# Optimization experiments

Hardware: AMD Instinct MI355X
Metric: run time of the kernel (lower is better)

The kernel has to match this reference:

```python
import jax, jax.numpy as jnp
import numpy as np

B, T, V, S, I, G = 2, 4096, 1024, 256, 2048, 128


def setup_inputs() -> dict:
    key = jax.random.key(0)
    ks = jax.random.split(key, 10)
    n = lambda k, shape, std: jax.random.normal(k, shape, dtype=jnp.float32) * std
    return {
        "x": jax.random.normal(ks[0], (B, T, V), dtype=jnp.float32),
        # shared CausalMemory projections (torch Linear weight layout [out,in])
        "Wq": n(ks[1], (S, V), 0.02),
        "Wk": n(ks[2], (S, V), 0.02),
        "Wv": n(ks[3], (S, V), 0.02),
        "Wo": n(ks[4], (V, S), 0.02),
        # Delta
        "delta_logits": jnp.full((V,), 4.0, dtype=jnp.float32),
        "delta_scale": jnp.float32(0.1),
        # Theta / Gamma decay params
        "theta_decay": jnp.float32(4.0),
        "theta_scale": jnp.float32(0.1),
        "gamma_decay": jnp.float32(1.0),
        "gamma_scale": jnp.float32(0.1),
        # Alpha gate
        "alpha_down": n(ks[5], (G, V), 0.02),
        "alpha_up": n(ks[6], (V, G), 0.01),
        "alpha_up_b": jnp.full((V,), 2.0, dtype=jnp.float32),
        # Beta MLP
        "beta_down": n(ks[7], (I, V), 0.02),
        "beta_up": n(ks[8], (V, I), 0.02),
        "beta_bias": jnp.zeros((I,), dtype=jnp.float32),
        "beta_scale": jnp.float32(0.1),
    }


def _rmsnorm(x):
    eps = jnp.finfo(x.dtype).eps
    return x * jax.lax.rsqrt(jnp.mean(x * x, axis=-1, keepdims=True) + eps)


def _delta(x, decay_logits, scale):
    # causal EMA via weighted cumsum, matching torch reference exactly
    t = x.shape[1]
    decay = jax.nn.sigmoid(decay_logits)
    log_decay = jnp.log(jnp.clip(decay, 1e-06))
    steps = jnp.arange(t, dtype=x.dtype)[::-1]            # [T]
    w = jnp.exp(steps[:, None] * log_decay[None, :])      # [T,V]
    cum = jnp.cumsum(x * w[None], axis=1)
    cum = jnp.concatenate([jnp.zeros_like(cum[:, :1]), cum[:, :-1]], axis=1)
    return cum / jnp.clip(w[None], 1e-08) * scale


def _memory(x, Wq, Wk, Wv, Wo, decay_logit, scale):
    t = x.shape[1]
    q = x @ Wq.T
    k = x @ Wk.T
    v = x @ Wv.T
    scores = jnp.einsum("btd,bsd->bts", q, k)             # [B,T,T]
    decay = jax.nn.sigmoid(decay_logit)
    pos = jnp.arange(t)
    diff = pos[None, :] - pos[:, None]                    # j - i
    w = decay ** jnp.clip(diff.astype(x.dtype) - 1.0, 0.0, None) * (diff > 0)
    retrieved = jnp.einsum("bts,bsd->btd", scores * w[None], v)
    return (retrieved @ Wo.T) * scale


def _alpha(x, down, up, up_b):
    gate = jax.nn.sigmoid((x @ down.T) @ up.T + up_b)
    return x * gate


def _beta(x, down, up, bias, scale):
    h = jax.nn.gelu(x @ down.T + bias, approximate=False)
    return (h @ up.T) * scale


def reference(x, Wq, Wk, Wv, Wo, delta_logits, delta_scale, theta_decay,
              theta_scale, gamma_decay, gamma_scale, alpha_down, alpha_up,
              alpha_up_b, beta_down, beta_up, beta_bias, beta_scale):
    x = x + _delta(_rmsnorm(x), delta_logits, delta_scale)
    x = x + _memory(_rmsnorm(x), Wq, Wk, Wv, Wo, theta_decay, theta_scale)
    x = _alpha(x, alpha_down, alpha_up, alpha_up_b)
    x = x + _beta(_rmsnorm(x), beta_down, beta_up, beta_bias, beta_scale)
    x = x + _memory(_rmsnorm(x), Wq, Wk, Wv, Wo, gamma_decay, gamma_scale)
    return x
```

## Files before the change

kernel.cpp:

```cpp
#include <hip/hip_runtime.h>

typedef __attribute__((ext_vector_type(8))) short s16x8;
typedef __attribute__((ext_vector_type(4))) float f32x4;
typedef unsigned short u16;

#define DEV __device__ __forceinline__

DEV u16 f2b(float f) {
  unsigned u = __builtin_bit_cast(unsigned, f);
  unsigned r = (u + 0x7FFFu + ((u >> 16) & 1u)) >> 16;
  return (u16)r;
}
DEV float b2f(u16 h) { return __builtin_bit_cast(float, (unsigned)h << 16); }
DEV f32x4 mfma16(s16x8 a, s16x8 b, f32x4 c) {
  return __builtin_amdgcn_mfma_f32_16x16x32_bf16(a, b, c, 0, 0, 0);
}
DEV float sigmoidf_(float x) { return 1.0f / (1.0f + expf(-x)); }

DEV void g2l16(const u16* g, u16* l) {
  __builtin_amdgcn_global_load_lds((const __attribute__((address_space(1))) void*)g,
                                   (__attribute__((address_space(3))) void*)l, 16, 0, 0);
}

#define BAR() __builtin_amdgcn_s_barrier()
#define WAITV8() asm volatile("s_waitcnt vmcnt(8)" ::: "memory")
#define WAITV4() asm volatile("s_waitcnt vmcnt(4)" ::: "memory")
#define WAITV0() asm volatile("s_waitcnt vmcnt(0)" ::: "memory")
#define WAITL0()                                         \
  do {                                                   \
    asm volatile("s_waitcnt lgkmcnt(0)" ::: "memory");   \
    __builtin_amdgcn_sched_barrier(0);                   \
  } while (0)

__global__ __launch_bounds__(256) void cast_all(
    const float* __restrict__ Wq, const float* __restrict__ Wk, const float* __restrict__ Wv,
    const float* __restrict__ Wo, const float* __restrict__ adw, const float* __restrict__ auw,
    const float* __restrict__ bdw, const float* __restrict__ buw,
    u16* __restrict__ Wqkvb, u16* __restrict__ Wob, u16* __restrict__ adb,
    u16* __restrict__ aub, u16* __restrict__ bdb, u16* __restrict__ bub) {
  const int b = blockIdx.x;
  const float* s;
  u16* d;
  int rb;
  if (b < 768) {
    s = (b < 256) ? Wq : (b < 512) ? Wk : Wv;
    rb = (b < 256) ? b : (b < 512) ? (b - 256) : (b - 512);
    d = Wqkvb + ((b < 256) ? 0 : (b < 512) ? 262144 : 524288);
  } else if (b < 1024) { s = Wo;  d = Wob; rb = b - 768; }
  else if (b < 1152)   { s = adw; d = adb; rb = b - 1024; }
  else if (b < 1280)   { s = auw; d = aub; rb = b - 1152; }
  else if (b < 3328)   { s = bdw; d = bdb; rb = b - 1280; }
  else                 { s = buw; d = bub; rb = b - 3328; }
  size_t i = ((size_t)rb * 256 + threadIdx.x) * 4;
  float4 v = *(const float4*)(s + i);
  ushort4 p; p.x = f2b(v.x); p.y = f2b(v.y); p.z = f2b(v.z); p.w = f2b(v.w);
  *(ushort4*)(d + i) = p;
}

__global__ __launch_bounds__(256) void rmsnorm_k(const float* __restrict__ x, u16* __restrict__ y) {
  const size_t row = blockIdx.x;
  const int tid = threadIdx.x;
  float4 v = ((const float4*)(x + row * 1024))[tid];
  float ss = v.x * v.x + v.y * v.y + v.z * v.z + v.w * v.w;
#pragma unroll
  for (int o = 32; o >= 1; o >>= 1) ss += __shfl_xor(ss, o);
  __shared__ float red[4];
  if ((tid & 63) == 0) red[tid >> 6] = ss;
  __syncthreads();
  float tot = red[0] + red[1] + red[2] + red[3];
  float rn = rsqrtf(tot * (1.0f / 1024.0f) + 1.1920929e-7f);
  ushort4 p;
  p.x = f2b(v.x * rn); p.y = f2b(v.y * rn); p.z = f2b(v.z * rn); p.w = f2b(v.w * rn);
  *(ushort4*)(y + row * 1024 + tid * 4) = p;
}

__global__ __launch_bounds__(256)
void delta_partial(const u16* __restrict__ y, const float* __restrict__ logits, float* __restrict__ Pp) {
  const int v = blockIdx.x * 256 + threadIdx.x;
  const int c = blockIdx.y, b = blockIdx.z;
  const float dec = sigmoidf_(logits[v]);
  const float ldc = logf(fmaxf(dec, 1e-6f));
  const u16* yp = y + ((size_t)b * 4096 + c * 128) * 1024 + v;
  float acc = 0.0f;
  for (int t = 0; t < 128; ++t) {
    float wgt = expf((float)(4095 - (c * 128 + t)) * ldc);
    acc += b2f(yp[(size_t)t * 1024]) * wgt;
  }
  Pp[((size_t)b * 32 + c) * 1024 + v] = acc;
}

__global__ __launch_bounds__(256) void delta_scan(float* __restrict__ Pp) {
  const int v = blockIdx.x * 256 + threadIdx.x;
  const int b = blockIdx.y;
  float run = 0.0f;
  for (int c = 0; c < 32; ++c) {
    size_t i = ((size_t)b * 32 + c) * 1024 + v;
    float t = Pp[i];
    Pp[i] = run;
    run += t;
  }
}

__global__ __launch_bounds__(256)
void delta_apply(const float* __restrict__ x0, const u16* __restrict__ y,
                 const float* __restrict__ logits, const float* __restrict__ scale_p,
                 const float* __restrict__ Pp, float* __restrict__ x1) {
  const int v = blockIdx.x * 256 + threadIdx.x;
  const int c = blockIdx.y, b = blockIdx.z;
  const float dec = sigmoidf_(logits[v]);
  const float ldc = logf(fmaxf(dec, 1e-6f));
  const float sc = scale_p[0];
  float carry = Pp[((size_t)b * 32 + c) * 1024 + v];
  size_t base = ((size_t)b * 4096 + c * 128) * 1024 + v;
  for (int t = 0; t < 128; ++t) {
    float wgt = expf((float)(4095 - (c * 128 + t)) * ldc);
    size_t idx = base + (size_t)t * 1024;
    x1[idx] = x0[idx] + carry / fmaxf(wgt, 1e-8f) * sc;
    carry += b2f(y[idx]) * wgt;
  }
}

template <int EPI>
__global__ __launch_bounds__(256, 2)
void pgemm(const u16* __restrict__ A, const u16* __restrict__ Bw,
           int M, int N, int K,
           u16* __restrict__ Cb,
           const float* __restrict__ Xin, float* __restrict__ Xout,
           u16* __restrict__ Xb16,
           const float* __restrict__ bias, const float* __restrict__ scale_p,
           u16* __restrict__ P1, u16* __restrict__ P2, u16* __restrict__ P3) {
  __shared__ u16 sm[32768];
  const int tid = threadIdx.x;
  const int wid = tid >> 6, lane = tid & 63;
  const int gx = gridDim.x;
  const int id = blockIdx.y * gx + blockIdx.x;
  const int q8 = (gx * gridDim.y) >> 3;
  const int nid = (id & 7) * q8 + (id >> 3);
  const int bx = nid % gx, by = nid / gx;
  const int n0 = bx * 128, m0 = by * 128;
  const int wm = (wid >> 1) * 64, wn = (wid & 1) * 64;
  const int lr = lane & 15, lkc = lane >> 4;
  const int sw = lr & 7;
  const int c0 = (lkc ^ sw) * 8, c1 = ((lkc + 4) ^ sw) * 8;
  const int NT = K >> 6;
  const int srow = lane >> 3;
  const int scol = ((lane & 7) ^ srow) * 8;
  const u16* Ag = A + (size_t)(m0 + wid * 8 + srow) * K + scol;
  const u16* Bg = Bw + (size_t)(n0 + wid * 8 + srow) * K + scol;
  u16* const AL0 = sm;          u16* const BL0 = sm + 8192;
  u16* const AL1 = sm + 16384;  u16* const BL1 = sm + 24576;

  f32x4 acc[4][4] = {};

  auto STA = [&](int tau) {
    const u16* g = Ag + (size_t)tau * 64;
    u16* l = ((tau & 1) ? AL1 : AL0) + wid * 512;
#pragma unroll
    for (int c = 0; c < 4; ++c) g2l16(g + (size_t)c * 32 * K, l + c * 2048);
  };
  auto STB = [&](int tau) {
    const u16* g = Bg + (size_t)tau * 64;
    u16* l = ((tau & 1) ? BL1 : BL0) + wid * 512;
#pragma unroll
    for (int c = 0; c < 4; ++c) g2l16(g + (size_t)c * 32 * K, l + c * 2048);
  };
  auto RDA = [&](int tau, s16x8 (&d)[4][2]) {
    const u16* Ab = (tau & 1) ? AL1 : AL0;
#pragma unroll
    for (int i = 0; i < 4; ++i) {
      int base = (wm + i * 16 + lr) * 64;
      d[i][0] = *(const s16x8*)&Ab[base + c0];
      d[i][1] = *(const s16x8*)&Ab[base + c1];
    }
  };
  auto RDB = [&](int tau, int h, s16x8 (&d)[2][2]) {
    const u16* Bb = (tau & 1) ? BL1 : BL0;
#pragma unroll
    for (int j = 0; j < 2; ++j) {
      int base = (wn + h * 32 + j * 16 + lr) * 64;
      d[j][0] = *(const s16x8*)&Bb[base + c0];
      d[j][1] = *(const s16x8*)&Bb[base + c1];
    }
  };
  auto MM = [&](s16x8 (&Ar)[4][2], s16x8 (&Br)[2][2], int jo) {
    __builtin_amdgcn_s_setprio(1);
#pragma unroll
    for (int i = 0; i < 4; ++i)
#pragma unroll
      for (int j = 0; j < 2; ++j) {
        acc[i][jo + j] = mfma16(Ar[i][0], Br[j][0], acc[i][jo + j]);
        acc[i][jo + j] = mfma16(Ar[i][1], Br[j][1], acc[i][jo + j]);
      }
    __builtin_amdgcn_s_setprio(0);
  };

  s16x8 Ae[4][2], Ao[4][2], B0r[2][2], B1r[2][2];
  STA(0); STB(0);
  if (NT > 1) { STA(1); STB(1); }
  WAITV8(); BAR();
  RDA(0, Ae); RDB(0, 0, B0r);

  for (int t = 0; t < NT; t += 2) {
    RDB(t, 1, B1r);
    if (t + 2 < NT) STA(t + 2);
    BAR(); WAITL0();
    MM(Ae, B0r, 0);
    BAR();
    if (t + 2 < NT) { STB(t + 2); WAITV8(); } else { WAITV0(); }
    BAR();
    if (t + 1 < NT) { RDA(t + 1, Ao); RDB(t + 1, 0, B0r); }
    WAITL0();
    MM(Ae, B1r, 2);
    BAR();
    if (t + 1 >= NT) break;
    RDB(t + 1, 1, B1r);
    if (t + 3 < NT) STA(t + 3);
    BAR(); WAITL0();
    MM(Ao, B0r, 0);
    BAR();
    if (t + 3 < NT) { STB(t + 3); WAITV8(); } else { WAITV0(); }
    BAR();
    if (t + 2 < NT) { RDA(t + 2, Ae); RDB(t + 2, 0, B0r); }
    WAITL0();
    MM(Ao, B1r, 2);
    BAR();
  }

  float* tl = (float*)(void*)sm + wid * 1088;

  if constexpr (EPI == 5) {
    if (bx < 4) {
      u16* dst = (bx < 2) ? Cb : P1;
      const int nb = (bx & 1) * 128;
#pragma unroll
      for (int i = 0; i < 4; ++i) {
#pragma unroll
        for (int j = 0; j < 4; ++j)
#pragma unroll
          for (int r = 0; r < 4; ++r)
            tl[(lkc * 4 + r) * 68 + j * 16 + lr] = acc[i][j][r];
#pragma unroll
        for (int p = 0; p < 4; ++p) {
          const int row = p * 4 + lkc, nl = lr * 4;
          f32x4 v = *(const f32x4*)&tl[row * 68 + nl];
          const int m = m0 + wm + i * 16 + row;
          ushort4 o = {f2b(v[0]), f2b(v[1]), f2b(v[2]), f2b(v[3])};
          *(ushort4*)&dst[(size_t)m * 256 + nb + wn + nl] = o;
        }
      }
      if (bx >= 2) {
        const float ld5 = logf(sigmoidf_(scale_p[0]));
        u16* CT = sm;
        __syncthreads();
#pragma unroll
        for (int i = 0; i < 4; ++i)
#pragma unroll
          for (int j = 0; j < 4; ++j)
#pragma unroll
            for (int r = 0; r < 4; ++r) {
              int ml = wm + i * 16 + lkc * 4 + r;
              int nl = wn + j * 16 + lr;
              float g = expf(ld5 * (float)(ml & 63));
              CT[nl * 136 + ml] = f2b(acc[i][j][r] * g);
            }
        __syncthreads();
        int d = tid >> 1, off = (tid & 1) * 64;
        size_t base = ((size_t)(m0 >> 12) * 256 + (bx - 2) * 128 + d) * 4096 + (m0 & 4095) + off;
#pragma unroll
        for (int p = 0; p < 8; ++p)
          *(uint4*)&P3[base + p * 8] = *(const uint4*)&CT[d * 136 + off + p * 8];
      }
    } else {
      u16* CT = sm;
      __syncthreads();
#pragma unroll
      for (int i = 0; i < 4; ++i)
#pragma unroll
        for (int j = 0; j < 4; ++j)
#pragma unroll
          for (int r = 0; r < 4; ++r) {
            int ml = wm + i * 16 + lkc * 4 + r;
            int nl = wn + j * 16 + lr;
            CT[nl * 136 + ml] = f2b(acc[i][j][r]);
          }
      __syncthreads();
      int d = tid >> 1, off = (tid & 1) * 64;
      size_t base = ((size_t)(m0 >> 12) * 256 + (bx - 4) * 128 + d) * 4096 + (m0 & 4095) + off;
#pragma unroll
      for (int p = 0; p < 8; ++p)
        *(uint4*)&P2[base + p * 8] = *(const uint4*)&CT[d * 136 + off + p * 8];
    }
  } else {
    const float sc = (EPI == 2) ? scale_p[0] : 0.0f;
#pragma unroll
    for (int i = 0; i < 4; ++i) {
#pragma unroll
      for (int j = 0; j < 4; ++j)
#pragma unroll
        for (int r = 0; r < 4; ++r)
          tl[(lkc * 4 + r) * 68 + j * 16 + lr] = acc[i][j][r];
#pragma unroll
      for (int p = 0; p < 4; ++p) {
        const int row = p * 4 + lkc, nl = lr * 4;
        f32x4 v = *(const f32x4*)&tl[row * 68 + nl];
        const int m = m0 + wm + i * 16 + row;
        const int n = n0 + wn + nl;
        const size_t idx = (size_t)m * N + n;
        if constexpr (EPI == 0) {
          ushort4 o = {f2b(v[0]), f2b(v[1]), f2b(v[2]), f2b(v[3])};
          *(ushort4*)&Cb[idx] = o;
        } else if constexpr (EPI == 2) {
          float4 x = *(const float4*)&Xin[idx];
          float4 o = {x.x + v[0] * sc, x.y + v[1] * sc, x.z + v[2] * sc, x.w + v[3] * sc};
          *(float4*)&Xout[idx] = o;
          if (Xb16) {
            ushort4 ob = {f2b(o.x), f2b(o.y), f2b(o.z), f2b(o.w)};
            *(ushort4*)&Xb16[idx] = ob;
          }
        } else if constexpr (EPI == 3) {
          float4 bb = *(const float4*)&bias[n];
          float g0 = v[0] + bb.x, g1 = v[1] + bb.y, g2 = v[2] + bb.z, g3 = v[3] + bb.w;
          ushort4 o;
          o.x = f2b(g0 * sigmoidf_(1.59576912f * fmaf(0.044715f * g0, g0 * g0, g0)));
          o.y = f2b(g1 * sigmoidf_(1.59576912f * fmaf(0.044715f * g1, g1 * g1, g1)));
          o.z = f2b(g2 * sigmoidf_(1.59576912f * fmaf(0.044715f * g2, g2 * g2, g2)));
          o.w = f2b(g3 * sigmoidf_(1.59576912f * fmaf(0.044715f * g3, g3 * g3, g3)));
          *(ushort4*)&Cb[idx] = o;
        } else {
          float4 bb = *(const float4*)&bias[n];
          float4 x = *(const float4*)&Xin[idx];
          float4 o = {x.x * sigmoidf_(v[0] + bb.x), x.y * sigmoidf_(v[1] + bb.y),
                      x.z * sigmoidf_(v[2] + bb.z), x.w * sigmoidf_(v[3] + bb.w)};
          *(float4*)&Xout[idx] = o;
        }
      }
    }
  }
}

__global__ __launch_bounds__(256, 2)
void chunk_G(const u16* __restrict__ vT, const u16* __restrict__ kTs, float* __restrict__ Gp) {
  __shared__ u16 sm2[16384];
  const int c = blockIdx.x, eh = blockIdx.y >> 1, dh = blockIdx.y & 1, b = blockIdx.z;
  const int tid = threadIdx.x, wid = tid >> 6, lane = tid & 63;
  u16* AL = sm2; u16* BL = sm2 + 8192;
  const u16* As = vT + (size_t)(b * 256 + eh * 128) * 4096 + c * 64;
  const u16* Bs = kTs + (size_t)(b * 256 + dh * 128) * 4096 + c * 64;
  const int r8 = lane >> 3, sc8 = ((lane & 7) ^ (lane >> 3)) * 8;
#pragma unroll
  for (int p = 0; p < 4; ++p) {
    int ch = p * 4 + wid;
    int row = ch * 8 + r8;
    g2l16(As + (size_t)row * 4096 + sc8, AL + ch * 512);
    g2l16(Bs + (size_t)row * 4096 + sc8, BL + ch * 512);
  }
  __syncthreads();
  const int wm = (wid >> 1) * 64, wn = (wid & 1) * 64;
  const int lr = lane & 15, lkc = lane >> 4, sw = lr & 7;
  const int c0 = (lkc ^ sw) * 8, c1 = ((lkc + 4) ^ sw) * 8;
  s16x8 af[4][2], bf[4][2];
#pragma unroll
  for (int i = 0; i < 4; ++i) {
    int ba = (wm + i * 16 + lr) * 64;
    af[i][0] = *(const s16x8*)&AL[ba + c0];
    af[i][1] = *(const s16x8*)&AL[ba + c1];
    int bb = (wn + i * 16 + lr) * 64;
    bf[i][0] = *(const s16x8*)&BL[bb + c0];
    bf[i][1] = *(const s16x8*)&BL[bb + c1];
  }
  f32x4 acc[4][4] = {};
#pragma unroll
  for (int i = 0; i < 4; ++i)
#pragma unroll
    for (int j = 0; j < 4; ++j) {
      acc[i][j] = mfma16(af[i][0], bf[j][0], acc[i][j]);
      acc[i][j] = mfma16(af[i][1], bf[j][1], acc[i][j]);
    }
  float* Gb = Gp + (size_t)(b * 64 + c) * 65536;
#pragma unroll
  for (int i = 0; i < 4; ++i)
#pragma unroll
    for (int j = 0; j < 4; ++j)
#pragma unroll
      for (int r = 0; r < 4; ++r) {
        int e = eh * 128 + wm + i * 16 + lkc * 4 + r;
        int d = dh * 128 + wn + j * 16 + lr;
        Gb[(size_t)e * 256 + d] = acc[i][j][r];
      }
}

__global__ __launch_bounds__(256)
void scan_M(const float* __restrict__ Gp, u16* __restrict__ Mb, const float* __restrict__ dlogit) {
  const int b = blockIdx.y;
  const size_t idx = ((size_t)blockIdx.x * 256 + threadIdx.x) * 4;
  const float ld = logf(sigmoidf_(dlogit[0]));
  const float g64 = expf(64.0f * ld);
  const float* G = Gp + (size_t)b * 64 * 65536 + idx;
  u16* M = Mb + (size_t)b * 64 * 65536 + idx;
  float4 m = {0.0f, 0.0f, 0.0f, 0.0f};
  *(ushort4*)(M + (size_t)63 * 65536) = (ushort4){0, 0, 0, 0};
  float4 g = *(const float4*)(G + (size_t)63 * 65536);
  for (int c = 62; c >= 0; --c) {
    float4 gn = {0.0f, 0.0f, 0.0f, 0.0f};
    if (c > 0) gn = *(const float4*)(G + (size_t)c * 65536);
    m.x = g.x + g64 * m.x; m.y = g.y + g64 * m.y;
    m.z = g.z + g64 * m.z; m.w = g.w + g64 * m.w;
    ushort4 o; o.x = f2b(m.x); o.y = f2b(m.y); o.z = f2b(m.z); o.w = f2b(m.w);
    *(ushort4*)(M + (size_t)c * 65536) = o;
    g = gn;
  }
}

__global__ __launch_bounds__(256, 2)
void chunk_R(const u16* __restrict__ q, const u16* __restrict__ k,
             const u16* __restrict__ vT, const u16* __restrict__ Mb,
             u16* __restrict__ R, const float* __restrict__ dlogit) {
  __shared__ u16 qL[16384];
  __shared__ u16 shA[16384];
  const int c = blockIdx.x, eh = blockIdx.y, b = blockIdx.z;
  const int tid = threadIdx.x, wid = tid >> 6, lane = tid & 63;
  const float ld = logf(sigmoidf_(dlogit[0]));
  const int r8 = lane >> 3, sc8 = ((lane & 7) ^ (lane >> 3)) * 8;
  const int lr = lane & 15, lkc = lane >> 4, g4 = lkc * 4;
  const int sw = lr & 7;
  const int c0 = (lkc ^ sw) * 8, c1 = ((lkc + 4) ^ sw) * 8;

  const u16* qsrc = q + ((size_t)b * 4096 + c * 64) * 256;
  const u16* ksrc = k + ((size_t)b * 4096 + c * 64) * 256;
  const u16* msrc = Mb + ((size_t)(b * 64 + c) * 256 + eh * 128) * 256;
  const u16* vsrc = vT + (size_t)(b * 256 + eh * 128) * 4096 + c * 64;

#pragma unroll
  for (int kt = 0; kt < 4; ++kt)
#pragma unroll
    for (int p = 0; p < 2; ++p) {
      int ch = p * 4 + wid;
      int row = ch * 8 + r8;
      g2l16(qsrc + (size_t)row * 256 + kt * 64 + sc8, qL + kt * 4096 + ch * 512);
    }
#pragma unroll
  for (int p = 0; p < 4; ++p) {
    int ch = p * 4 + wid;
    int row = ch * 8 + r8;
    g2l16(msrc + (size_t)row * 256 + sc8, shA + ch * 512);
  }
  f32x4 accx[4][2] = {};
  for (int dt = 0; dt < 4; ++dt) {
    if (dt < 3) {
      u16* dst = shA + ((dt + 1) & 1) * 8192;
#pragma unroll
      for (int p = 0; p < 4; ++p) {
        int ch = p * 4 + wid;
        int row = ch * 8 + r8;
        g2l16(msrc + (size_t)row * 256 + (dt + 1) * 64 + sc8, dst + ch * 512);
      }
      WAITV4();
    } else {
      WAITV0();
    }
    BAR();
    const u16* mt = shA + (dt & 1) * 8192;
    const u16* qt = qL + dt * 4096;
    s16x8 aq[4][2], bm[2][2];
#pragma unroll
    for (int i = 0; i < 4; ++i) {
      int ba = (i * 16 + lr) * 64;
      aq[i][0] = *(const s16x8*)&qt[ba + c0];
      aq[i][1] = *(const s16x8*)&qt[ba + c1];
    }
#pragma unroll
    for (int j = 0; j < 2; ++j) {
      int ba = (wid * 32 + j * 16 + lr) * 64;
      bm[j][0] = *(const s16x8*)&mt[ba + c0];
      bm[j][1] = *(const s16x8*)&mt[ba + c1];
    }
#pragma unroll
    for (int i = 0; i < 4; ++i)
#pragma unroll
      for (int j = 0; j < 2; ++j) {
        accx[i][j] = mfma16(aq[i][0], bm[j][0], accx[i][j]);
        accx[i][j] = mfma16(aq[i][1], bm[j][1], accx[i][j]);
      }
    BAR();
  }
#pragma unroll
  for (int kt = 0; kt < 4; ++kt)
#pragma unroll
    for (int p = 0; p < 2; ++p) {
      int ch = p * 4 + wid;
      int row = ch * 8 + r8;
      g2l16(ksrc + (size_t)row * 256 + kt * 64 + sc8, shA + kt * 4096 + ch * 512);
    }
  __syncthreads();
  f32x4 accs[4] = {};
#pragma unroll
  for (int kt = 0; kt < 4; ++kt) {
    const u16* qt = qL + kt * 4096;
    const u16* klt = shA + kt * 4096;
    s16x8 aq[4][2], bk[2];
#pragma unroll
    for (int i = 0; i < 4; ++i) {
      int ba = (i * 16 + lr) * 64;
      aq[i][0] = *(const s16x8*)&qt[ba + c0];
      aq[i][1] = *(const s16x8*)&qt[ba + c1];
    }
    {
      int ba = (wid * 16 + lr) * 64;
      bk[0] = *(const s16x8*)&klt[ba + c0];
      bk[1] = *(const s16x8*)&klt[ba + c1];
    }
#pragma unroll
    for (int i = 0; i < 4; ++i) {
      accs[i] = mfma16(aq[i][0], bk[0], accs[i]);
      accs[i] = mfma16(aq[i][1], bk[1], accs[i]);
    }
  }
  __syncthreads();
  u16* PL = shA;
  u16* vTL = shA + 4608;
#pragma unroll
  for (int p = 0; p < 4; ++p) {
    int ch = p * 4 + wid;
    int row = ch * 8 + r8;
    g2l16(vsrc + (size_t)row * 4096 + sc8, vTL + ch * 512);
  }
#pragma unroll
  for (int i = 0; i < 4; ++i)
#pragma unroll
    for (int r = 0; r < 4; ++r) {
      int gi = i * 16 + g4 + r;
      int gj = wid * 16 + lr;
      float pw = (gj > gi) ? expf(ld * (float)(gj - gi - 1)) : 0.0f;
      PL[gi * 72 + gj] = f2b(accs[i][r] * pw);
    }
  __syncthreads();
  f32x4 acci[4][2] = {};
  {
    s16x8 pa[4][2], bv[2][2];
#pragma unroll
    for (int i = 0; i < 4; ++i) {
      pa[i][0] = *(const s16x8*)&PL[(i * 16 + lr) * 72 + lkc * 8];
      pa[i][1] = *(const s16x8*)&PL[(i * 16 + lr) * 72 + 32 + lkc * 8];
    }
#pragma unroll
    for (int j = 0; j < 2; ++j) {
      int ba = (wid * 32 + j * 16 + lr) * 64;
      bv[j][0] = *(const s16x8*)&vTL[ba + c0];
      bv[j][1] = *(const s16x8*)&vTL[ba + c1];
    }
#pragma unroll
    for (int i = 0; i < 4; ++i)
#pragma unroll
      for (int j = 0; j < 2; ++j) {
        acci[i][j] = mfma16(pa[i][0], bv[j][0], acci[i][j]);
        acci[i][j] = mfma16(pa[i][1], bv[j][1], acci[i][j]);
      }
  }
  u16* Ro = R + ((size_t)b * 4096 + c * 64) * 256 + eh * 128;
#pragma unroll
  for (int i = 0; i < 4; ++i)
#pragma unroll
    for (int r = 0; r < 4; ++r) {
      int gi = i * 16 + g4 + r;
      float xf = expf(ld * (float)(63 - gi));
#pragma unroll
      for (int j = 0; j < 2; ++j) {
        int ge = wid * 32 + j * 16 + lr;
        Ro[(size_t)gi * 256 + ge] = f2b(acci[i][j][r] + xf * accx[i][j][r]);
      }
    }
}

extern "C" void kernel_launch(void* const* d_in, const int* in_sizes, int n_in,
                              void* d_out, int out_size, void* d_ws, size_t ws_size,
                              hipStream_t stream) {
  const float* x0 = (const float*)d_in[0];
  const float* Wq = (const float*)d_in[1];
  const float* Wk = (const float*)d_in[2];
  const float* Wv = (const float*)d_in[3];
  const float* Wo = (const float*)d_in[4];
  const float* dlog = (const float*)d_in[5];
  const float* dscale = (const float*)d_in[6];
  const float* th_dec = (const float*)d_in[7];
  const float* th_sc = (const float*)d_in[8];
  const float* ga_dec = (const float*)d_in[9];
  const float* ga_sc = (const float*)d_in[10];
  const float* adw = (const float*)d_in[11];
  const float* auw = (const float*)d_in[12];
  const float* a_upb = (const float*)d_in[13];
  const float* bdw = (const float*)d_in[14];
  const float* buw = (const float*)d_in[15];
  const float* bbias = (const float*)d_in[16];
  const float* bscale = (const float*)d_in[17];

  char* w = (char*)d_ws;
  float* xA = (float*)w;
  u16* y = (u16*)(w + 33554432);
  u16* xb = (u16*)(w + 50331648);
  u16* qb = (u16*)(w + 67108864);
  u16* kb = (u16*)(w + 71303168);
  u16* vT = (u16*)(w + 75497472);
  u16* Rb = (u16*)(w + 79691776);
  u16* gb = (u16*)(w + 83886080);
  u16* hb = (u16*)(w + 85983232);
  float* Gp = (float*)hb;
  u16* Mbuf = y;
  u16* kTs = xb;
  float* Pp = (float*)(w + 119537664);
  u16* Wqkvb = (u16*)(w + 119799808);
  u16* Wob = (u16*)(w + 121372672);
  u16* adb = (u16*)(w + 121896960);
  u16* aub = (u16*)(w + 122159104);
  u16* bdb = (u16*)(w + 122421248);
  u16* bub = (u16*)(w + 126615552);
  float* xB = (float*)d_out;

  cast_all<<<5376, 256, 0, stream>>>(Wq, Wk, Wv, Wo, adw, auw, bdw, buw,
                                     Wqkvb, Wob, adb, aub, bdb, bub);

  rmsnorm_k<<<8192, 256, 0, stream>>>(x0, y);
  delta_partial<<<dim3(4, 32, 2), 256, 0, stream>>>(y, dlog, Pp);
  delta_scan<<<dim3(4, 2), 256, 0, stream>>>(Pp);
  delta_apply<<<dim3(4, 32, 2), 256, 0, stream>>>(x0, y, dlog, dscale, Pp, xA);

  rmsnorm_k<<<8192, 256, 0, stream>>>(xA, y);
  pgemm<5><<<dim3(6, 64), 256, 0, stream>>>(y, Wqkvb, 8192, 768, 1024, qb, nullptr, nullptr, nullptr, nullptr, th_dec, kb, vT, kTs);
  chunk_G<<<dim3(64, 4, 2), 256, 0, stream>>>(vT, kTs, Gp);
  scan_M<<<dim3(64, 2), 256, 0, stream>>>(Gp, Mbuf, th_dec);
  chunk_R<<<dim3(64, 2, 2), 256, 0, stream>>>(qb, kb, vT, Mbuf, Rb, th_dec);
  pgemm<2><<<dim3(8, 64), 256, 0, stream>>>(Rb, Wob, 8192, 1024, 256, nullptr, xA, xB, xb, nullptr, th_sc, nullptr, nullptr, nullptr);

  pgemm<0><<<dim3(1, 64), 256, 0, stream>>>(xb, adb, 8192, 128, 1024, gb, nullptr, nullptr, nullptr, nullptr, nullptr, nullptr, nullptr, nullptr);
  pgemm<4><<<dim3(8, 64), 256, 0, stream>>>(gb, aub, 8192, 1024, 128, nullptr, xB, xA, nullptr, a_upb, nullptr, nullptr, nullptr, nullptr);

  rmsnorm_k<<<8192, 256, 0, stream>>>(xA, y);
  pgemm<3><<<dim3(16, 64), 256, 0, stream>>>(y, bdb, 8192, 2048, 1024, hb, nullptr, nullptr, nullptr, bbias, nullptr, nullptr, nullptr, nullptr);
  pgemm<2><<<dim3(8, 64), 256, 0, stream>>>(hb, bub, 8192, 1024, 2048, nullptr, xA, xB, nullptr, nullptr, bscale, nullptr, nullptr, nullptr);

  rmsnorm_k<<<8192, 256, 0, stream>>>(xB, y);
  pgemm<5><<<dim3(6, 64), 256, 0, stream>>>(y, Wqkvb, 8192, 768, 1024, qb, nullptr, nullptr, nullptr, nullptr, ga_dec, kb, vT, kTs);
  chunk_G<<<dim3(64, 4, 2), 256, 0, stream>>>(vT, kTs, Gp);
  scan_M<<<dim3(64, 2), 256, 0, stream>>>(Gp, Mbuf, ga_dec);
  chunk_R<<<dim3(64, 2, 2), 256, 0, stream>>>(qb, kb, vT, Mbuf, Rb, ga_dec);
  pgemm<2><<<dim3(8, 64), 256, 0, stream>>>(Rb, Wob, 8192, 1024, 256, nullptr, xB, xB, nullptr, nullptr, ga_sc, nullptr, nullptr, nullptr);
}
```

Measured before the change: 333.0 us.

## Use 8-wave 256x128 GEMM tiles and recurrent decay weights in delta kernels

Most GEMMs move to a new 512-thread kernel that computes a 256x128 output tile with 8 waves sharing one B tile. This halves B traffic per output and changes the LDS layout and pipeline schedule. The original 256-thread kernel is kept only for the N=128 alpha-down GEMM. Separately, the delta partial and apply kernels replace a per-step expf with multiplicative recurrences for the decay weight and its inverse, which adds a risk of accumulated rounding error and a different clamp behaviour.

```diff
diff --git a/kernel.cpp b/kernel.cpp
--- a/kernel.cpp
+++ b/kernel.cpp
@@ -80,11 +80,13 @@
   const int c = blockIdx.y, b = blockIdx.z;
   const float dec = sigmoidf_(logits[v]);
   const float ldc = logf(fmaxf(dec, 1e-6f));
+  const float dc = expf(ldc);
   const u16* yp = y + ((size_t)b * 4096 + c * 128) * 1024 + v;
+  float wv = expf((float)(4095 - (c * 128 + 127)) * ldc);
   float acc = 0.0f;
-  for (int t = 0; t < 128; ++t) {
-    float wgt = expf((float)(4095 - (c * 128 + t)) * ldc);
-    acc += b2f(yp[(size_t)t * 1024]) * wgt;
+  for (int t = 127; t >= 0; --t) {
+    acc += b2f(yp[(size_t)t * 1024]) * wv;
+    wv *= dc;
   }
   Pp[((size_t)b * 32 + c) * 1024 + v] = acc;
 }
@@ -109,27 +111,32 @@
   const int c = blockIdx.y, b = blockIdx.z;
   const float dec = sigmoidf_(logits[v]);
   const float ldc = logf(fmaxf(dec, 1e-6f));
+  const float dc = expf(ldc);
+  const float invd = expf(-ldc);
   const float sc = scale_p[0];
+  float wv = expf((float)(4095 - c * 128) * ldc);
+  float iw = expf(-(float)(4095 - c * 128) * ldc);
   float carry = Pp[((size_t)b * 32 + c) * 1024 + v];
   size_t base = ((size_t)b * 4096 + c * 128) * 1024 + v;
   for (int t = 0; t < 128; ++t) {
-    float wgt = expf((float)(4095 - (c * 128 + t)) * ldc);
     size_t idx = base + (size_t)t * 1024;
-    x1[idx] = x0[idx] + carry / fmaxf(wgt, 1e-8f) * sc;
-    carry += b2f(y[idx]) * wgt;
+    x1[idx] = x0[idx] + carry * fminf(iw, 1e8f) * sc;
+    carry += b2f(y[idx]) * wv;
+    wv *= invd;
+    iw *= dc;
   }
 }
 
 template <int EPI>
-__global__ __launch_bounds__(256, 2)
-void pgemm(const u16* __restrict__ A, const u16* __restrict__ Bw,
-           int M, int N, int K,
-           u16* __restrict__ Cb,
-           const float* __restrict__ Xin, float* __restrict__ Xout,
-           u16* __restrict__ Xb16,
-           const float* __restrict__ bias, const float* __restrict__ scale_p,
-           u16* __restrict__ P1, u16* __restrict__ P2, u16* __restrict__ P3) {
-  __shared__ u16 sm[32768];
+__global__ __launch_bounds__(512, 2)
+void pgemm8(const u16* __restrict__ A, const u16* __restrict__ Bw,
+            int M, int N, int K,
+            u16* __restrict__ Cb,
+            const float* __restrict__ Xin, float* __restrict__ Xout,
+            u16* __restrict__ Xb16,
+            const float* __restrict__ bias, const float* __restrict__ scale_p,
+            u16* __restrict__ P1, u16* __restrict__ P2, u16* __restrict__ P3) {
+  __shared__ u16 sm[49152];
   const int tid = threadIdx.x;
   const int wid = tid >> 6, lane = tid & 63;
   const int gx = gridDim.x;
@@ -137,7 +144,7 @@
   const int q8 = (gx * gridDim.y) >> 3;
   const int nid = (id & 7) * q8 + (id >> 3);
   const int bx = nid % gx, by = nid / gx;
-  const int n0 = bx * 128, m0 = by * 128;
+  const int n0 = bx * 128, m0 = by * 256;
   const int wm = (wid >> 1) * 64, wn = (wid & 1) * 64;
   const int lr = lane & 15, lkc = lane >> 4;
   const int sw = lr & 7;
@@ -147,25 +154,23 @@
   const int scol = ((lane & 7) ^ srow) * 8;
   const u16* Ag = A + (size_t)(m0 + wid * 8 + srow) * K + scol;
   const u16* Bg = Bw + (size_t)(n0 + wid * 8 + srow) * K + scol;
-  u16* const AL0 = sm;          u16* const BL0 = sm + 8192;
-  u16* const AL1 = sm + 16384;  u16* const BL1 = sm + 24576;
 
   f32x4 acc[4][4] = {};
 
-  auto STA = [&](int tau) {
-    const u16* g = Ag + (size_t)tau * 64;
-    u16* l = ((tau & 1) ? AL1 : AL0) + wid * 512;
-#pragma unroll
-    for (int c = 0; c < 4; ++c) g2l16(g + (size_t)c * 32 * K, l + c * 2048);
+  auto STA = [&](int tau, int h) {
+    const u16* g = Ag + (size_t)(h * 128) * K + (size_t)tau * 64;
+    u16* l = sm + ((tau & 1) ? 16384 : 0) + h * 8192 + wid * 512;
+    g2l16(g, l);
+    g2l16(g + (size_t)64 * K, l + 4096);
   };
   auto STB = [&](int tau) {
     const u16* g = Bg + (size_t)tau * 64;
-    u16* l = ((tau & 1) ? BL1 : BL0) + wid * 512;
-#pragma unroll
-    for (int c = 0; c < 4; ++c) g2l16(g + (size_t)c * 32 * K, l + c * 2048);
+    u16* l = sm + ((tau & 1) ? 40960 : 32768) + wid * 512;
+    g2l16(g, l);
+    g2l16(g + (size_t)64 * K, l + 4096);
   };
   auto RDA = [&](int tau, s16x8 (&d)[4][2]) {
-    const u16* Ab = (tau & 1) ? AL1 : AL0;
+    const u16* Ab = sm + ((tau & 1) ? 16384 : 0);
 #pragma unroll
     for (int i = 0; i < 4; ++i) {
       int base = (wm + i * 16 + lr) * 64;
@@ -173,56 +178,54 @@
       d[i][1] = *(const s16x8*)&Ab[base + c1];
     }
   };
-  auto RDB = [&](int tau, int h, s16x8 (&d)[2][2]) {
-    const u16* Bb = (tau & 1) ? BL1 : BL0;
+  auto RDB = [&](int tau, int jp, s16x8 (&d)[2][2]) {
+    const u16* Bb = sm + ((tau & 1) ? 40960 : 32768);
 #pragma unroll
     for (int j = 0; j < 2; ++j) {
-      int base = (wn + h * 32 + j * 16 + lr) * 64;
+      int base = (wn + (jp * 2 + j) * 16 + lr) * 64;
       d[j][0] = *(const s16x8*)&Bb[base + c0];
       d[j][1] = *(const s16x8*)&Bb[base + c1];
     }
   };
-  auto MM = [&](s16x8 (&Ar)[4][2], s16x8 (&Br)[2][2], int jo) {
+  auto MM = [&](s16x8 (&Ar)[4][2], s16x8 (&Br)[2][2], int jp) {
     __builtin_amdgcn_s_setprio(1);
 #pragma unroll
     for (int i = 0; i < 4; ++i)
 #pragma unroll
       for (int j = 0; j < 2; ++j) {
-        acc[i][jo + j] = mfma16(Ar[i][0], Br[j][0], acc[i][jo + j]);
-        acc[i][jo + j] = mfma16(Ar[i][1], Br[j][1], acc[i][jo + j]);
+        acc[i][jp * 2 + j] = mfma16(Ar[i][0], Br[j][0], acc[i][jp * 2 + j]);
+        acc[i][jp * 2 + j] = mfma16(Ar[i][1], Br[j][1], acc[i][jp * 2 + j]);
       }
     __builtin_amdgcn_s_setprio(0);
   };
 
-  s16x8 Ae[4][2], Ao[4][2], B0r[2][2], B1r[2][2];
-  STA(0); STB(0);
-  if (NT > 1) { STA(1); STB(1); }
-  WAITV8(); BAR();
-  RDA(0, Ae); RDB(0, 0, B0r);
+  s16x8 a[4][2], b[2][2];
+  STA(0, 0); STA(0, 1); STB(0); STA(1, 0); STA(1, 1);
+  WAITV4(); BAR();
 
   for (int t = 0; t < NT; t += 2) {
-    RDB(t, 1, B1r);
-    if (t + 2 < NT) STA(t + 2);
+    const bool last = (t + 2 >= NT);
+    RDA(t, a); RDB(t, 0, b);
+    STB(t + 1);
     BAR(); WAITL0();
-    MM(Ae, B0r, 0);
-    BAR();
-    if (t + 2 < NT) { STB(t + 2); WAITV8(); } else { WAITV0(); }
-    BAR();
-    if (t + 1 < NT) { RDA(t + 1, Ao); RDB(t + 1, 0, B0r); }
-    WAITL0();
-    MM(Ae, B1r, 2);
-    BAR();
-    if (t + 1 >= NT) break;
-    RDB(t + 1, 1, B1r);
-    if (t + 3 < NT) STA(t + 3);
+    MM(a, b, 0);
+    BAR();
+    RDB(t, 1, b);
+    if (!last) { STA(t + 2, 0); STA(t + 2, 1); }
     BAR(); WAITL0();
-    MM(Ao, B0r, 0);
-    BAR();
-    if (t + 3 < NT) { STB(t + 3); WAITV8(); } else { WAITV0(); }
-    BAR();
-    if (t + 2 < NT) { RDA(t + 2, Ae); RDB(t + 2, 0, B0r); }
-    WAITL0();
-    MM(Ao, B1r, 2);
+    MM(a, b, 1);
+    if (!last) { WAITV4(); } else { WAITV0(); }
+    BAR();
+    RDA(t + 1, a); RDB(t + 1, 0, b);
+    if (!last) STB(t + 2);
+    BAR(); WAITL0();
+    MM(a, b, 0);
+    BAR();
+    RDB(t + 1, 1, b);
+    if (!last) { STA(t + 3, 0); STA(t + 3, 1); }
+    BAR(); WAITL0();
+    MM(a, b, 1);
+    if (!last) WAITV4();
     BAR();
   }
 
@@ -261,14 +264,14 @@
               int ml = wm + i * 16 + lkc * 4 + r;
               int nl = wn + j * 16 + lr;
               float g = expf(ld5 * (float)(ml & 63));
-              CT[nl * 136 + ml] = f2b(acc[i][j][r] * g);
+              CT[nl * 264 + ml] = f2b(acc[i][j][r] * g);
             }
         __syncthreads();
-        int d = tid >> 1, off = (tid & 1) * 64;
-        size_t base = ((size_t)(m0 >> 12) * 256 + (bx - 2) * 128 + d) * 4096 + (m0 & 4095) + off;
+        int rw = tid >> 2, off = (tid & 3) * 64;
+        size_t base = ((size_t)(m0 >> 12) * 256 + (bx - 2) * 128 + rw) * 4096 + (m0 & 4095) + off;
 #pragma unroll
         for (int p = 0; p < 8; ++p)
-          *(uint4*)&P3[base + p * 8] = *(const uint4*)&CT[d * 136 + off + p * 8];
+          *(uint4*)&P3[base + p * 8] = *(const uint4*)&CT[rw * 264 + off + p * 8];
       }
     } else {
       u16* CT = sm;
@@ -281,14 +284,14 @@
           for (int r = 0; r < 4; ++r) {
             int ml = wm + i * 16 + lkc * 4 + r;
             int nl = wn + j * 16 + lr;
-            CT[nl * 136 + ml] = f2b(acc[i][j][r]);
+            CT[nl * 264 + ml] = f2b(acc[i][j][r]);
           }
       __syncthreads();
-      int d = tid >> 1, off = (tid & 1) * 64;
-      size_t base = ((size_t)(m0 >> 12) * 256 + (bx - 4) * 128 + d) * 4096 + (m0 & 4095) + off;
+      int rw = tid >> 2, off = (tid & 3) * 64;
+      size_t base = ((size_t)(m0 >> 12) * 256 + (bx - 4) * 128 + rw) * 4096 + (m0 & 4095) + off;
 #pragma unroll
       for (int p = 0; p < 8; ++p)
-        *(uint4*)&P2[base + p * 8] = *(const uint4*)&CT[d * 136 + off + p * 8];
+        *(uint4*)&P2[base + p * 8] = *(const uint4*)&CT[rw * 264 + off + p * 8];
     }
   } else {
     const float sc = (EPI == 2) ? scale_p[0] : 0.0f;
@@ -338,6 +341,126 @@
   }
 }
 
+template <int EPI>
+__global__ __launch_bounds__(256, 2)
+void pgemm(const u16* __restrict__ A, const u16* __restrict__ Bw,
+           int M, int N, int K, u16* __restrict__ Cb) {
+  __shared__ u16 sm[32768];
+  const int tid = threadIdx.x;
+  const int wid = tid >> 6, lane = tid & 63;
+  const int gx = gridDim.x;
+  const int id = blockIdx.y * gx + blockIdx.x;
+  const int q8 = (gx * gridDim.y) >> 3;
+  const int nid = (id & 7) * q8 + (id >> 3);
+  const int bx = nid % gx, by = nid / gx;
+  const int n0 = bx * 128, m0 = by * 128;
+  const int wm = (wid >> 1) * 64, wn = (wid & 1) * 64;
+  const int lr = lane & 15, lkc = lane >> 4;
+  const int sw = lr & 7;
+  const int c0 = (lkc ^ sw) * 8, c1 = ((lkc + 4) ^ sw) * 8;
+  const int NT = K >> 6;
+  const int srow = lane >> 3;
+  const int scol = ((lane & 7) ^ srow) * 8;
+  const u16* Ag = A + (size_t)(m0 + wid * 8 + srow) * K + scol;
+  const u16* Bg = Bw + (size_t)(n0 + wid * 8 + srow) * K + scol;
+  u16* const AL0 = sm;          u16* const BL0 = sm + 8192;
+  u16* const AL1 = sm + 16384;  u16* const BL1 = sm + 24576;
+
+  f32x4 acc[4][4] = {};
+
+  auto STA = [&](int tau) {
+    const u16* g = Ag + (size_t)tau * 64;
+    u16* l = ((tau & 1) ? AL1 : AL0) + wid * 512;
+#pragma unroll
+    for (int c = 0; c < 4; ++c) g2l16(g + (size_t)c * 32 * K, l + c * 2048);
+  };
+  auto STB = [&](int tau) {
+    const u16* g = Bg + (size_t)tau * 64;
+    u16* l = ((tau & 1) ? BL1 : BL0) + wid * 512;
+#pragma unroll
+    for (int c = 0; c < 4; ++c) g2l16(g + (size_t)c * 32 * K, l + c * 2048);
+  };
+  auto RDA = [&](int tau, s16x8 (&d)[4][2]) {
+    const u16* Ab = (tau & 1) ? AL1 : AL0;
+#pragma unroll
+    for (int i = 0; i < 4; ++i) {
+      int base = (wm + i * 16 + lr) * 64;
+      d[i][0] = *(const s16x8*)&Ab[base + c0];
+      d[i][1] = *(const s16x8*)&Ab[base + c1];
+    }
+  };
+  auto RDB = [&](int tau, int h, s16x8 (&d)[2][2]) {
+    const u16* Bb = (tau & 1) ? BL1 : BL0;
+#pragma unroll
+    for (int j = 0; j < 2; ++j) {
+      int base = (wn + h * 32 + j * 16 + lr) * 64;
+      d[j][0] = *(const s16x8*)&Bb[base + c0];
+      d[j][1] = *(const s16x8*)&Bb[base + c1];
+    }
+  };
+  auto MM = [&](s16x8 (&Ar)[4][2], s16x8 (&Br)[2][2], int jo) {
+    __builtin_amdgcn_s_setprio(1);
+#pragma unroll
+    for (int i = 0; i < 4; ++i)
+#pragma unroll
+      for (int j = 0; j < 2; ++j) {
+        acc[i][jo + j] = mfma16(Ar[i][0], Br[j][0], acc[i][jo + j]);
+        acc[i][jo + j] = mfma16(Ar[i][1], Br[j][1], acc[i][jo + j]);
+      }
+    __builtin_amdgcn_s_setprio(0);
+  };
+
+  s16x8 Ae[4][2], Ao[4][2], B0r[2][2], B1r[2][2];
+  STA(0); STB(0);
+  if (NT > 1) { STA(1); STB(1); }
+  WAITV8(); BAR();
+  RDA(0, Ae); RDB(0, 0, B0r);
+
+  for (int t = 0; t < NT; t += 2) {
+    RDB(t, 1, B1r);
+    if (t + 2 < NT) STA(t + 2);
+    BAR(); WAITL0();
+    MM(Ae, B0r, 0);
+    BAR();
+    if (t + 2 < NT) { STB(t + 2); WAITV8(); } else { WAITV0(); }
+    BAR();
+    if (t + 1 < NT) { RDA(t + 1, Ao); RDB(t + 1, 0, B0r); }
+    WAITL0();
+    MM(Ae, B1r, 2);
+    BAR();
+    if (t + 1 >= NT) break;
+    RDB(t + 1, 1, B1r);
+    if (t + 3 < NT) STA(t + 3);
+    BAR(); WAITL0();
+    MM(Ao, B0r, 0);
+    BAR();
+    if (t + 3 < NT) { STB(t + 3); WAITV8(); } else { WAITV0(); }
+    BAR();
+    if (t + 2 < NT) { RDA(t + 2, Ae); RDB(t + 2, 0, B0r); }
+    WAITL0();
+    MM(Ao, B1r, 2);
+    BAR();
+  }
+
+  float* tl = (float*)(void*)sm + wid * 1088;
+#pragma unroll
+  for (int i = 0; i < 4; ++i) {
+#pragma unroll
+    for (int j = 0; j < 4; ++j)
+#pragma unroll
+      for (int r = 0; r < 4; ++r)
+        tl[(lkc * 4 + r) * 68 + j * 16 + lr] = acc[i][j][r];
+#pragma unroll
+    for (int p = 0; p < 4; ++p) {
+      const int row = p * 4 + lkc, nl = lr * 4;
+      f32x4 v = *(const f32x4*)&tl[row * 68 + nl];
+      const int m = m0 + wm + i * 16 + row;
+      ushort4 o = {f2b(v[0]), f2b(v[1]), f2b(v[2]), f2b(v[3])};
+      *(ushort4*)&Cb[(size_t)m * N + n0 + wn + nl] = o;
+    }
+  }
+}
+
 __global__ __launch_bounds__(256, 2)
 void chunk_G(const u16* __restrict__ vT, const u16* __restrict__ kTs, float* __restrict__ Gp) {
   __shared__ u16 sm2[16384];
@@ -624,23 +747,23 @@
   delta_apply<<<dim3(4, 32, 2), 256, 0, stream>>>(x0, y, dlog, dscale, Pp, xA);
 
   rmsnorm_k<<<8192, 256, 0, stream>>>(xA, y);
-  pgemm<5><<<dim3(6, 64), 256, 0, stream>>>(y, Wqkvb, 8192, 768, 1024, qb, nullptr, nullptr, nullptr, nullptr, th_dec, kb, vT, kTs);
+  pgemm8<5><<<dim3(6, 32), 512, 0, stream>>>(y, Wqkvb, 8192, 768, 1024, qb, nullptr, nullptr, nullptr, nullptr, th_dec, kb, vT, kTs);
   chunk_G<<<dim3(64, 4, 2), 256, 0, stream>>>(vT, kTs, Gp);
   scan_M<<<dim3(64, 2), 256, 0, stream>>>(Gp, Mbuf, th_dec);
   chunk_R<<<dim3(64, 2, 2), 256, 0, stream>>>(qb, kb, vT, Mbuf, Rb, th_dec);
-  pgemm<2><<<dim3(8, 64), 256, 0, stream>>>(Rb, Wob, 8192, 1024, 256, nullptr, xA, xB, xb, nullptr, th_sc, nullptr, nullptr, nullptr);
-
-  pgemm<0><<<dim3(1, 64), 256, 0, stream>>>(xb, adb, 8192, 128, 1024, gb, nullptr, nullptr, nullptr, nullptr, nullptr, nullptr, nullptr, nullptr);
-  pgemm<4><<<dim3(8, 64), 256, 0, stream>>>(gb, aub, 8192, 1024, 128, nullptr, xB, xA, nullptr, a_upb, nullptr, nullptr, nullptr, nullptr);
+  pgemm8<2><<<dim3(8, 32), 512, 0, stream>>>(Rb, Wob, 8192, 1024, 256, nullptr, xA, xB, xb, nullptr, th_sc, nullptr, nullptr, nullptr);
+
+  pgemm<0><<<dim3(1, 64), 256, 0, stream>>>(xb, adb, 8192, 128, 1024, gb);
+  pgemm8<4><<<dim3(8, 32), 512, 0, stream>>>(gb, aub, 8192, 1024, 128, nullptr, xB, xA, nullptr, a_upb, nullptr, nullptr, nullptr, nullptr);
 
   rmsnorm_k<<<8192, 256, 0, stream>>>(xA, y);
-  pgemm<3><<<dim3(16, 64), 256, 0, stream>>>(y, bdb, 8192, 2048, 1024, hb, nullptr, nullptr, nullptr, bbias, nullptr, nullptr, nullptr, nullptr);
-  pgemm<2><<<dim3(8, 64), 256, 0, stream>>>(hb, bub, 8192, 1024, 2048, nullptr, xA, xB, nullptr, nullptr, bscale, nullptr, nullptr, nullptr);
+  pgemm8<3><<<dim3(16, 32), 512, 0, stream>>>(y, bdb, 8192, 2048, 1024, hb, nullptr, nullptr, nullptr, bbias, nullptr, nullptr, nullptr, nullptr);
+  pgemm8<2><<<dim3(8, 32), 512, 0, stream>>>(hb, bub, 8192, 1024, 2048, nullptr, xA, xB, nullptr, nullptr, bscale, nullptr, nullptr, nullptr);
 
   rmsnorm_k<<<8192, 256, 0, stream>>>(xB, y);
-  pgemm<5><<<dim3(6, 64), 256, 0, stream>>>(y, Wqkvb, 8192, 768, 1024, qb, nullptr, nullptr, nullptr, nullptr, ga_dec, kb, vT, kTs);
+  pgemm8<5><<<dim3(6, 32), 512, 0, stream>>>(y, Wqkvb, 8192, 768, 1024, qb, nullptr, nullptr, nullptr, nullptr, ga_dec, kb, vT, kTs);
   chunk_G<<<dim3(64, 4, 2), 256, 0, stream>>>(vT, kTs, Gp);
   scan_M<<<dim3(64, 2), 256, 0, stream>>>(Gp, Mbuf, ga_dec);
   chunk_R<<<dim3(64, 2, 2), 256, 0, stream>>>(qb, kb, vT, Mbuf, Rb, ga_dec);
-  pgemm<2><<<dim3(8, 64), 256, 0, stream>>>(Rb, Wob, 8192, 1024, 256, nullptr, xB, xB, nullptr, nullptr, ga_sc, nullptr, nullptr, nullptr);
-}
+  pgemm8<2><<<dim3(8, 32), 512, 0, stream>>>(Rb, Wob, 8192, 1024, 256, nullptr, xB, xB, nullptr, nullptr, ga_sc, nullptr, nullptr, nullptr);
+}
```

Measured after the change: 340.3 us. 1.02x slower.
